# Kernel tuning notes

Hardware: AMD Instinct MI355X
Metric: run time of the kernel (lower is better)

The kernel has to match this reference:

```python
import jax, jax.numpy as jnp
import numpy as np


def setup_inputs() -> dict:
    key = jax.random.key(0)
    ks = jax.random.split(key, 4)
    B, S, D, E = 8, 4096, 2048, 64
    scale = 1.0 / np.sqrt(D)
    return {
        "x": jax.random.normal(ks[0], (B, S, D), dtype=jnp.float32),
        "W_route": jax.random.normal(ks[1], (E, D), dtype=jnp.float32) * scale,
        "b_route": jnp.zeros((E,), dtype=jnp.float32),
        "W_noise": jax.random.normal(ks[2], (E, D), dtype=jnp.float32) * scale,
        "b_noise": jnp.zeros((E,), dtype=jnp.float32),
        "noise_eps": jax.random.normal(ks[3], (B, S, E), dtype=jnp.float32),
    }


TOP_K = 2


def reference(x, W_route, b_route, W_noise, b_noise, noise_eps):
    # Dual linear projections: [B,S,D] @ [D,E] -> [B,S,E]
    logits = jnp.einsum("bsd,ed->bse", x, W_route) + b_route
    noise_logits = jnp.einsum("bsd,ed->bse", x, W_noise) + b_noise
    noisy_logits = logits + noise_eps * jax.nn.softplus(noise_logits)

    B, S, E = noisy_logits.shape
    flat = noisy_logits.reshape(B * S, E)
    top_vals, top_idx = jax.lax.top_k(flat, TOP_K)  # [N,K]

    # Scatter top-k values into -inf background, then softmax over experts.
    neg_inf = jnp.full_like(flat, -jnp.inf)
    rows = jnp.arange(B * S)[:, None]
    sparse = neg_inf.at[rows, top_idx].set(top_vals)
    router_output = jax.nn.softmax(sparse, axis=-1).reshape(B, S, E)
    indices = top_idx.reshape(B, S, TOP_K)
    return router_output, indices
```

## Files before the change

### kernel.cpp

```cpp
#include <hip/hip_runtime.h>
#include <math.h>

typedef _Float16 f16;
typedef __attribute__((ext_vector_type(8))) _Float16 half8;
typedef __attribute__((ext_vector_type(4))) float f32x4;

#define NEXP 64
#define TM 64
#define L_STRIDE 132

__device__ __forceinline__ float softplus_f(float x) {
    return fmaxf(x, 0.0f) + log1pf(expf(-fabsf(x)));
}

__device__ __forceinline__ void lds_dma16(const void* g, void* l) {
    __builtin_amdgcn_global_load_lds(
        (const __attribute__((address_space(1))) unsigned int*)g,
        (__attribute__((address_space(3))) unsigned int*)l, 16, 0, 0);
}

__device__ __forceinline__ void cvt_split(const float4 a, const float4 b,
                                          half8& hv, half8& lv) {
    const float vv[8] = {a.x, a.y, a.z, a.w, b.x, b.y, b.z, b.w};
#pragma unroll
    for (int j = 0; j < 8; ++j) {
        const f16 h = (f16)vv[j];
        hv[j] = h;
        lv[j] = (f16)((vv[j] - (float)h) * 4096.0f);
    }
}

__global__ void wsplit_kernel(const float* __restrict__ Wr,
                              const float* __restrict__ Wn,
                              f16* __restrict__ ws, int D) {
    const int per_col = D >> 3;
    const int t = blockIdx.x * blockDim.x + threadIdx.x;
    const int col = t / per_col;
    const int k0  = (t - col * per_col) * 8;
    if (col >= 128) return;
    const float* src = (col < NEXP) ? &Wr[(size_t)col * D] : &Wn[(size_t)(col - NEXP) * D];
    const float4 v0 = *(const float4*)&src[k0];
    const float4 v1 = *(const float4*)&src[k0 + 4];
    half8 hi, lo;
    cvt_split(v0, v1, hi, lo);
    const int kc = k0 >> 5, q = (k0 >> 3) & 3;
    const size_t base = (size_t)kc * 8192 + (size_t)q * 1024 + (size_t)col * 8;
    *(half8*)&ws[base]        = hi;
    *(half8*)&ws[base + 4096] = lo;
}

__global__ __launch_bounds__(256, 3)
void router_mfma_kernel(const float* __restrict__ x,
                        const f16* __restrict__ wsW,
                        const float* __restrict__ br,
                        const float* __restrict__ bn,
                        const float* __restrict__ eps,
                        float* __restrict__ out,
                        int N, int D) {
    __shared__ union alignas(16) {
        struct { f16 B[2][8192]; f16 A[2][4096]; } st;
        float L[TM][L_STRIDE];
    } sm;
    __shared__ float biasLDS[128];
    __shared__ float p1s[TM], p2s[TM];
    __shared__ int   i1s[TM], i2s[TM];

    const int tid  = threadIdx.x;
    const int lane = tid & 63;
    const int w    = tid >> 6;
    const int rowbase = blockIdx.x * TM;
    const int wr = w & 1, wc = w >> 1;
    const int quad = lane >> 4;
    const int l16  = lane & 15;

    if (tid < 128) biasLDS[tid] = (tid < NEXP) ? br[tid] : bn[tid - NEXP];

    f32x4 accM[2][4], accC[2][4];
#pragma unroll
    for (int i = 0; i < 2; ++i)
#pragma unroll
        for (int j = 0; j < 4; ++j) {
            accM[i][j] = (f32x4){0.f, 0.f, 0.f, 0.f};
            accC[i][j] = (f32x4){0.f, 0.f, 0.f, 0.f};
        }

    const int sr = tid >> 2;
    const int sq = tid & 3;
    const float* xrow = &x[(size_t)(rowbase + sr) * D + sq * 8];
    const int nkc = D >> 5;

    {
        const char* gsrc = (const char*)wsW + (size_t)0 * 16384 + w * 4096 + lane * 16;
        char* ldst = (char*)&sm.st.B[0][0] + w * 4096;
#pragma unroll
        for (int i = 0; i < 4; ++i) lds_dma16(gsrc + i * 1024, ldst + i * 1024);
        const float4 a0 = *(const float4*)&xrow[0];
        const float4 a1 = *(const float4*)&xrow[4];
        half8 hv, lv;
        cvt_split(a0, a1, hv, lv);
        *(half8*)&sm.st.A[0][sq * 512 + sr * 8]        = hv;
        *(half8*)&sm.st.A[0][2048 + sq * 512 + sr * 8] = lv;
    }
    float4 v0 = *(const float4*)&xrow[32];
    float4 v1 = *(const float4*)&xrow[36];
    __syncthreads();

#pragma unroll 2
    for (int kc = 0; kc < nkc; ++kc) {
        const int cur = kc & 1, nxt = cur ^ 1;

        if (kc + 1 < nkc) {
            const char* gsrc = (const char*)wsW + (size_t)(kc + 1) * 16384 + w * 4096 + lane * 16;
            char* ldst = (char*)&sm.st.B[nxt][0] + w * 4096;
#pragma unroll
            for (int i = 0; i < 4; ++i) lds_dma16(gsrc + i * 1024, ldst + i * 1024);
            half8 hv, lv;
            cvt_split(v0, v1, hv, lv);
            *(half8*)&sm.st.A[nxt][sq * 512 + sr * 8]        = hv;
            *(half8*)&sm.st.A[nxt][2048 + sq * 512 + sr * 8] = lv;
        }
        if (kc + 2 < nkc) {
            v0 = *(const float4*)&xrow[(kc + 2) * 32];
            v1 = *(const float4*)&xrow[(kc + 2) * 32 + 4];
        }

        half8 ah[2], al[2], bh[4], bl[4];
#pragma unroll
        for (int rt = 0; rt < 2; ++rt) {
            const int r = (wr * 32 + rt * 16 + l16) * 8;
            ah[rt] = *(const half8*)&sm.st.A[cur][quad * 512 + r];
            al[rt] = *(const half8*)&sm.st.A[cur][2048 + quad * 512 + r];
        }
#pragma unroll
        for (int ct = 0; ct < 4; ++ct) {
            const int c = (wc * 64 + ct * 16 + l16) * 8;
            bh[ct] = *(const half8*)&sm.st.B[cur][quad * 1024 + c];
            bl[ct] = *(const half8*)&sm.st.B[cur][4096 + quad * 1024 + c];
        }

#pragma unroll
        for (int rt = 0; rt < 2; ++rt)
#pragma unroll
            for (int ct = 0; ct < 4; ++ct) {
                accM[rt][ct] = __builtin_amdgcn_mfma_f32_16x16x32_f16(ah[rt], bh[ct], accM[rt][ct], 0, 0, 0);
                accC[rt][ct] = __builtin_amdgcn_mfma_f32_16x16x32_f16(al[rt], bh[ct], accC[rt][ct], 0, 0, 0);
                accC[rt][ct] = __builtin_amdgcn_mfma_f32_16x16x32_f16(ah[rt], bl[ct], accC[rt][ct], 0, 0, 0);
            }
        __syncthreads();
    }

#pragma unroll
    for (int rt = 0; rt < 2; ++rt)
#pragma unroll
        for (int ct = 0; ct < 4; ++ct) {
            const int row = wr * 32 + rt * 16 + quad * 4;
            const int col = wc * 64 + ct * 16 + l16;
            const float bcol = biasLDS[col];
#pragma unroll
            for (int rg = 0; rg < 4; ++rg)
                sm.L[row + rg][col] = accM[rt][ct][rg] + accC[rt][ct][rg] * (1.0f / 4096.0f) + bcol;
        }
    __syncthreads();

#pragma unroll
    for (int t = 0; t < 4; ++t) {
        const int f   = tid * 4 + t * 1024;
        const int row = f >> 6;
        const int e0  = f & 63;
        const float4 ev = *(const float4*)&eps[(size_t)(rowbase + row) * NEXP + e0];
        const float evs[4] = {ev.x, ev.y, ev.z, ev.w};
#pragma unroll
        for (int j = 0; j < 4; ++j) {
            const float lg = sm.L[row][e0 + j];
            const float nz = sm.L[row][NEXP + e0 + j];
            sm.L[row][e0 + j] = fmaf(evs[j], softplus_f(nz), lg);
        }
    }
    __syncthreads();

    if (tid < TM) {
        const int r = tid;
        float v1t = -INFINITY, v2t = -INFINITY;
        int i1 = 0, i2 = 0;
#pragma unroll 8
        for (int e = 0; e < NEXP; ++e) {
            const float v = sm.L[r][e];
            if (v > v1t) { v2t = v1t; i2 = i1; v1t = v; i1 = e; }
            else if (v > v2t) { v2t = v; i2 = e; }
        }
        const float z = expf(v2t - v1t);
        const float s = 1.0f + z;
        p1s[r] = 1.0f / s;
        p2s[r] = z / s;
        i1s[r] = i1;
        i2s[r] = i2;
        float* oidx = out + (size_t)N * NEXP + (size_t)(rowbase + r) * 2;
        oidx[0] = (float)i1;
        oidx[1] = (float)i2;
    }
    __syncthreads();

    {
        const int r = tid >> 2;
        const int g = tid & 3;
        const float pa = p1s[r], pb = p2s[r];
        const int i1 = i1s[r], i2 = i2s[r];
        float* orow = out + (size_t)(rowbase + r) * NEXP;
#pragma unroll
        for (int t = 0; t < 4; ++t) {
            const int e0 = g * 16 + t * 4;
            float4 o;
            o.x = (e0 + 0 == i1) ? pa : ((e0 + 0 == i2) ? pb : 0.0f);
            o.y = (e0 + 1 == i1) ? pa : ((e0 + 1 == i2) ? pb : 0.0f);
            o.z = (e0 + 2 == i1) ? pa : ((e0 + 2 == i2) ? pb : 0.0f);
            o.w = (e0 + 3 == i1) ? pa : ((e0 + 3 == i2) ? pb : 0.0f);
            *(float4*)&orow[e0] = o;
        }
    }
}

#define BK 32
#define XS_STRIDE (TM + 4)
#define WS_STRIDE (128 + 4)

__global__ __launch_bounds__(256, 2)
void noisy_topk_router_kernel(const float* __restrict__ x,
                              const float* __restrict__ Wr,
                              const float* __restrict__ br,
                              const float* __restrict__ Wn,
                              const float* __restrict__ bn,
                              const float* __restrict__ eps,
                              float* __restrict__ out,
                              int N, int D) {
    __shared__ union alignas(16) {
        struct {
            float Xs[BK][XS_STRIDE];
            float Ws[BK][WS_STRIDE];
        } st;
        float L[TM][L_STRIDE];
    } sm;
    __shared__ float p1s[TM], p2s[TM];
    __shared__ int   i1s[TM], i2s[TM];

    const int tid = threadIdx.x;
    const int rowbase = blockIdx.x * TM;
    const int r0 = (tid >> 5) * 8;
    const int c0 = (tid & 31) * 4;

    float acc[8][4];
#pragma unroll
    for (int i = 0; i < 8; ++i)
#pragma unroll
        for (int j = 0; j < 4; ++j) acc[i][j] = 0.0f;

    const int q  = tid & 7;
    const int rr = tid >> 3;

    for (int k0 = 0; k0 < D; k0 += BK) {
#pragma unroll
        for (int i = 0; i < 2; ++i) {
            const int row = rr + 32 * i;
            const float4 xv = *(const float4*)&x[(size_t)(rowbase + row) * D + k0 + q * 4];
            sm.st.Xs[q * 4 + 0][row] = xv.x;
            sm.st.Xs[q * 4 + 1][row] = xv.y;
            sm.st.Xs[q * 4 + 2][row] = xv.z;
            sm.st.Xs[q * 4 + 3][row] = xv.w;
            const float4 wv = *(const float4*)&Wr[(size_t)row * D + k0 + q * 4];
            sm.st.Ws[q * 4 + 0][row] = wv.x;
            sm.st.Ws[q * 4 + 1][row] = wv.y;
            sm.st.Ws[q * 4 + 2][row] = wv.z;
            sm.st.Ws[q * 4 + 3][row] = wv.w;
            const float4 nv = *(const float4*)&Wn[(size_t)row * D + k0 + q * 4];
            sm.st.Ws[q * 4 + 0][NEXP + row] = nv.x;
            sm.st.Ws[q * 4 + 1][NEXP + row] = nv.y;
            sm.st.Ws[q * 4 + 2][NEXP + row] = nv.z;
            sm.st.Ws[q * 4 + 3][NEXP + row] = nv.w;
        }
        __syncthreads();
#pragma unroll 4
        for (int kk = 0; kk < BK; ++kk) {
            const float4 xa = *(const float4*)&sm.st.Xs[kk][r0];
            const float4 xb = *(const float4*)&sm.st.Xs[kk][r0 + 4];
            const float4 wv = *(const float4*)&sm.st.Ws[kk][c0];
            const float xs[8] = {xa.x, xa.y, xa.z, xa.w, xb.x, xb.y, xb.z, xb.w};
            const float ws[4] = {wv.x, wv.y, wv.z, wv.w};
#pragma unroll
            for (int i = 0; i < 8; ++i)
#pragma unroll
                for (int j = 0; j < 4; ++j)
                    acc[i][j] = fmaf(xs[i], ws[j], acc[i][j]);
        }
        __syncthreads();
    }
    {
        const float4 bv = (c0 < NEXP) ? *(const float4*)&br[c0]
                                      : *(const float4*)&bn[c0 - NEXP];
#pragma unroll
        for (int i = 0; i < 8; ++i) {
            float4 o;
            o.x = acc[i][0] + bv.x;
            o.y = acc[i][1] + bv.y;
            o.z = acc[i][2] + bv.z;
            o.w = acc[i][3] + bv.w;
            *(float4*)&sm.L[r0 + i][c0] = o;
        }
    }
    __syncthreads();
#pragma unroll
    for (int t = 0; t < 4; ++t) {
        const int f   = tid * 4 + t * 1024;
        const int row = f >> 6;
        const int e0  = f & 63;
        const float4 ev = *(const float4*)&eps[(size_t)(rowbase + row) * NEXP + e0];
        const float evs[4] = {ev.x, ev.y, ev.z, ev.w};
#pragma unroll
        for (int j = 0; j < 4; ++j) {
            const float lg = sm.L[row][e0 + j];
            const float nz = sm.L[row][NEXP + e0 + j];
            sm.L[row][e0 + j] = fmaf(evs[j], softplus_f(nz), lg);
        }
    }
    __syncthreads();
    if (tid < TM) {
        const int r = tid;
        float v1 = -INFINITY, v2 = -INFINITY;
        int i1 = 0, i2 = 0;
#pragma unroll 8
        for (int e = 0; e < NEXP; ++e) {
            const float v = sm.L[r][e];
            if (v > v1) { v2 = v1; i2 = i1; v1 = v; i1 = e; }
            else if (v > v2) { v2 = v; i2 = e; }
        }
        const float z = expf(v2 - v1);
        const float s = 1.0f + z;
        p1s[r] = 1.0f / s;
        p2s[r] = z / s;
        i1s[r] = i1;
        i2s[r] = i2;
        float* oidx = out + (size_t)N * NEXP + (size_t)(rowbase + r) * 2;
        oidx[0] = (float)i1;
        oidx[1] = (float)i2;
    }
    __syncthreads();
    {
        const int r = tid >> 2;
        const int g = tid & 3;
        const float pa = p1s[r], pb = p2s[r];
        const int i1 = i1s[r], i2 = i2s[r];
        float* orow = out + (size_t)(rowbase + r) * NEXP;
#pragma unroll
        for (int t = 0; t < 4; ++t) {
            const int e0 = g * 16 + t * 4;
            float4 o;
            o.x = (e0 + 0 == i1) ? pa : ((e0 + 0 == i2) ? pb : 0.0f);
            o.y = (e0 + 1 == i1) ? pa : ((e0 + 1 == i2) ? pb : 0.0f);
            o.z = (e0 + 2 == i1) ? pa : ((e0 + 2 == i2) ? pb : 0.0f);
            o.w = (e0 + 3 == i1) ? pa : ((e0 + 3 == i2) ? pb : 0.0f);
            *(float4*)&orow[e0] = o;
        }
    }
}

extern "C" void kernel_launch(void* const* d_in, const int* in_sizes, int n_in,
                              void* d_out, int out_size, void* d_ws, size_t ws_size,
                              hipStream_t stream) {
    const float* x   = (const float*)d_in[0];
    const float* Wr  = (const float*)d_in[1];
    const float* br  = (const float*)d_in[2];
    const float* Wn  = (const float*)d_in[3];
    const float* bn  = (const float*)d_in[4];
    const float* eps = (const float*)d_in[5];
    float* out = (float*)d_out;

    const int E = in_sizes[2];
    const int D = in_sizes[1] / E;
    const int N = in_sizes[0] / D;

    const size_t ws_needed = (size_t)128 * D * 2 * sizeof(f16);
    const bool fast = (E == 64) && (D == 2048) && (N % TM == 0) && (ws_size >= ws_needed);

    if (fast) {
        const int pre_threads = 128 * (D / 8);
        wsplit_kernel<<<(pre_threads + 255) / 256, 256, 0, stream>>>(Wr, Wn, (f16*)d_ws, D);
        router_mfma_kernel<<<N / TM, 256, 0, stream>>>(x, (const f16*)d_ws, br, bn, eps, out, N, D);
    } else {
        noisy_topk_router_kernel<<<N / TM, 256, 0, stream>>>(x, Wr, br, Wn, bn, eps, out, N, D);
    }
}
```

Measured before the change: 429.0 us.

## Load MFMA operands directly from global memory, dropping LDS staging

The GEMM main loop stops staging x and the split-f16 weights through double-buffered LDS. Each wave now loads its own A rows and B fragments straight from global memory into registers, converts x to hi/lo f16 in registers, and issues the MFMAs. The per-iteration __syncthreads is replaced by a plain barrier every eight chunks to keep waves roughly in step. This removes LDS traffic and barrier stalls, but the two waves sharing a row block each load the same x rows and every wave rereads the weights from global/L2, which raises global load pressure.

```diff
diff --git a/kernel.cpp b/kernel.cpp
--- a/kernel.cpp
+++ b/kernel.cpp
@@ -11,12 +11,6 @@
 
 __device__ __forceinline__ float softplus_f(float x) {
     return fmaxf(x, 0.0f) + log1pf(expf(-fabsf(x)));
-}
-
-__device__ __forceinline__ void lds_dma16(const void* g, void* l) {
-    __builtin_amdgcn_global_load_lds(
-        (const __attribute__((address_space(1))) unsigned int*)g,
-        (__attribute__((address_space(3))) unsigned int*)l, 16, 0, 0);
 }
 
 __device__ __forceinline__ void cvt_split(const float4 a, const float4 b,
@@ -57,10 +51,7 @@
                         const float* __restrict__ eps,
                         float* __restrict__ out,
                         int N, int D) {
-    __shared__ union alignas(16) {
-        struct { f16 B[2][8192]; f16 A[2][4096]; } st;
-        float L[TM][L_STRIDE];
-    } sm;
+    __shared__ float L[TM][L_STRIDE];
     __shared__ float biasLDS[128];
     __shared__ float p1s[TM], p2s[TM];
     __shared__ int   i1s[TM], i2s[TM];
@@ -84,59 +75,42 @@
             accC[i][j] = (f32x4){0.f, 0.f, 0.f, 0.f};
         }
 
-    const int sr = tid >> 2;
-    const int sq = tid & 3;
-    const float* xrow = &x[(size_t)(rowbase + sr) * D + sq * 8];
+    const float* xp0 = &x[(size_t)(rowbase + wr * 32 + l16) * D + quad * 8];
+    const float* xp1 = xp0 + (size_t)16 * D;
+    const f16* bp0 = wsW + quad * 1024 + (wc * 64 + l16) * 8;
+    const f16* bp1 = bp0 + 4096;
+
     const int nkc = D >> 5;
 
-    {
-        const char* gsrc = (const char*)wsW + (size_t)0 * 16384 + w * 4096 + lane * 16;
-        char* ldst = (char*)&sm.st.B[0][0] + w * 4096;
-#pragma unroll
-        for (int i = 0; i < 4; ++i) lds_dma16(gsrc + i * 1024, ldst + i * 1024);
-        const float4 a0 = *(const float4*)&xrow[0];
-        const float4 a1 = *(const float4*)&xrow[4];
-        half8 hv, lv;
-        cvt_split(a0, a1, hv, lv);
-        *(half8*)&sm.st.A[0][sq * 512 + sr * 8]        = hv;
-        *(half8*)&sm.st.A[0][2048 + sq * 512 + sr * 8] = lv;
-    }
-    float4 v0 = *(const float4*)&xrow[32];
-    float4 v1 = *(const float4*)&xrow[36];
-    __syncthreads();
+    float4 a0n = *(const float4*)(xp0);
+    float4 a1n = *(const float4*)(xp0 + 4);
+    float4 a2n = *(const float4*)(xp1);
+    float4 a3n = *(const float4*)(xp1 + 4);
 
 #pragma unroll 2
     for (int kc = 0; kc < nkc; ++kc) {
-        const int cur = kc & 1, nxt = cur ^ 1;
-
+        const float4 a0 = a0n, a1 = a1n, a2 = a2n, a3 = a3n;
         if (kc + 1 < nkc) {
-            const char* gsrc = (const char*)wsW + (size_t)(kc + 1) * 16384 + w * 4096 + lane * 16;
-            char* ldst = (char*)&sm.st.B[nxt][0] + w * 4096;
-#pragma unroll
-            for (int i = 0; i < 4; ++i) lds_dma16(gsrc + i * 1024, ldst + i * 1024);
-            half8 hv, lv;
-            cvt_split(v0, v1, hv, lv);
-            *(half8*)&sm.st.A[nxt][sq * 512 + sr * 8]        = hv;
-            *(half8*)&sm.st.A[nxt][2048 + sq * 512 + sr * 8] = lv;
-        }
-        if (kc + 2 < nkc) {
-            v0 = *(const float4*)&xrow[(kc + 2) * 32];
-            v1 = *(const float4*)&xrow[(kc + 2) * 32 + 4];
-        }
-
-        half8 ah[2], al[2], bh[4], bl[4];
-#pragma unroll
-        for (int rt = 0; rt < 2; ++rt) {
-            const int r = (wr * 32 + rt * 16 + l16) * 8;
-            ah[rt] = *(const half8*)&sm.st.A[cur][quad * 512 + r];
-            al[rt] = *(const half8*)&sm.st.A[cur][2048 + quad * 512 + r];
-        }
+            const float* p0 = xp0 + (size_t)(kc + 1) * 32;
+            const float* p1 = xp1 + (size_t)(kc + 1) * 32;
+            a0n = *(const float4*)(p0);
+            a1n = *(const float4*)(p0 + 4);
+            a2n = *(const float4*)(p1);
+            a3n = *(const float4*)(p1 + 4);
+        }
+
+        const f16* b0 = bp0 + (size_t)kc * 8192;
+        const f16* b1 = bp1 + (size_t)kc * 8192;
+        half8 bh[4], bl[4];
 #pragma unroll
         for (int ct = 0; ct < 4; ++ct) {
-            const int c = (wc * 64 + ct * 16 + l16) * 8;
-            bh[ct] = *(const half8*)&sm.st.B[cur][quad * 1024 + c];
-            bl[ct] = *(const half8*)&sm.st.B[cur][4096 + quad * 1024 + c];
-        }
+            bh[ct] = *(const half8*)(b0 + ct * 128);
+            bl[ct] = *(const half8*)(b1 + ct * 128);
+        }
+
+        half8 ah[2], al[2];
+        cvt_split(a0, a1, ah[0], al[0]);
+        cvt_split(a2, a3, ah[1], al[1]);
 
 #pragma unroll
         for (int rt = 0; rt < 2; ++rt)
@@ -146,8 +120,10 @@
                 accC[rt][ct] = __builtin_amdgcn_mfma_f32_16x16x32_f16(al[rt], bh[ct], accC[rt][ct], 0, 0, 0);
                 accC[rt][ct] = __builtin_amdgcn_mfma_f32_16x16x32_f16(ah[rt], bl[ct], accC[rt][ct], 0, 0, 0);
             }
-        __syncthreads();
-    }
+
+        if ((kc & 7) == 7) __builtin_amdgcn_s_barrier();
+    }
+    __syncthreads();
 
 #pragma unroll
     for (int rt = 0; rt < 2; ++rt)
@@ -158,7 +134,7 @@
             const float bcol = biasLDS[col];
 #pragma unroll
             for (int rg = 0; rg < 4; ++rg)
-                sm.L[row + rg][col] = accM[rt][ct][rg] + accC[rt][ct][rg] * (1.0f / 4096.0f) + bcol;
+                L[row + rg][col] = accM[rt][ct][rg] + accC[rt][ct][rg] * (1.0f / 4096.0f) + bcol;
         }
     __syncthreads();
 
@@ -171,9 +147,9 @@
         const float evs[4] = {ev.x, ev.y, ev.z, ev.w};
 #pragma unroll
         for (int j = 0; j < 4; ++j) {
-            const float lg = sm.L[row][e0 + j];
-            const float nz = sm.L[row][NEXP + e0 + j];
-            sm.L[row][e0 + j] = fmaf(evs[j], softplus_f(nz), lg);
+            const float lg = L[row][e0 + j];
+            const float nz = L[row][NEXP + e0 + j];
+            L[row][e0 + j] = fmaf(evs[j], softplus_f(nz), lg);
         }
     }
     __syncthreads();
@@ -184,7 +160,7 @@
         int i1 = 0, i2 = 0;
 #pragma unroll 8
         for (int e = 0; e < NEXP; ++e) {
-            const float v = sm.L[r][e];
+            const float v = L[r][e];
             if (v > v1t) { v2t = v1t; i2 = i1; v1t = v; i1 = e; }
             else if (v > v2t) { v2t = v; i2 = e; }
         }
```

After: 432.8 us. Within noise of the previous version (+0.9%).
